# Kernel optimization log

Hardware: AMD Instinct MI355X
Metric: run time of the kernel (lower is better)

## Reference

```python
import jax, jax.numpy as jnp
import numpy as np

DIM = 1024
D_STATE = 16
D_CONV = 4
EXPAND = 2
D_INNER = EXPAND * DIM          # 2048
DT_RANK = -(-DIM // 16)        # ceil(dim/16) = 64
BATCH = 2
SEQ = 1024


def activation_quant(x):
    # int8 fake-quant with STE, per-row scale (matches torch source incl. grad paths)
    scale = 127.0 / jnp.clip(jnp.max(jnp.abs(x), axis=-1, keepdims=True), 1e-5)
    s = x * scale
    q = jnp.clip(jnp.round(s), -128.0, 127.0)
    return (jax.lax.stop_gradient(q - s) + s) / scale


def weight_quant(w):
    # ternary quant {-1,0,1} with straight-through estimator (grad = identity)
    scale = jnp.clip(jnp.mean(jnp.abs(w)), 1e-5)
    wq = jnp.clip(jnp.round(w / scale), -1.0, 1.0)
    return w + jax.lax.stop_gradient(wq - w)


def bit_linear(x, w):
    # LayerNorm (no affine, eps=1e-5) -> act quant -> ternary-weight matmul
    mu = jnp.mean(x, axis=-1, keepdims=True)
    var = jnp.mean((x - mu) ** 2, axis=-1, keepdims=True)
    xn = (x - mu) * jax.lax.rsqrt(var + 1e-5)
    return activation_quant(xn) @ weight_quant(w).T


def rms_norm(x, w, eps=1e-6):
    return w * (x * jax.lax.rsqrt(jnp.mean(x * x, axis=-1, keepdims=True) + eps))


def selective_scan(x, delta, A, Bm, Cm, D, z):
    # x, delta: [b,l,d]; Bm, Cm: [b,l,n]; A: [d,n]; D: [d]; z: [b,l,d]
    def step(h, inp):
        x_t, d_t, B_t, C_t = inp              # [b,d],[b,d],[b,n],[b,n]
        dA = jnp.exp(d_t[:, :, None] * A)     # [b,d,n]
        h = dA * h + d_t[:, :, None] * B_t[:, None, :] * x_t[:, :, None]
        y = jnp.einsum('bdn,bn->bd', h, C_t)
        return h, y

    h0 = jnp.zeros((x.shape[0], A.shape[0], A.shape[1]), x.dtype)
    seq_first = lambda t: jnp.moveaxis(t, 1, 0)
    _, ys = jax.lax.scan(step, h0, (seq_first(x), seq_first(delta), seq_first(Bm), seq_first(Cm)))
    y = jnp.moveaxis(ys, 0, 1) + x * D
    return y * jax.nn.silu(z)


def mamba_forward(hidden_states, rms_w, in_proj_w, x_proj_w, out_proj_w,
                  conv_w, conv_b, dt_proj_w, dt_proj_b, A_log, D):
    b, l, _ = hidden_states.shape
    h = rms_norm(hidden_states, rms_w)
    xz = bit_linear(h, in_proj_w)                      # [b,l,2*d_inner]
    x, z = jnp.split(xz, 2, axis=-1)

    # depthwise causal conv1d + bias
    xc = jnp.moveaxis(x, 1, 2)                         # [b,d_inner,l]
    xc = jax.lax.conv_general_dilated(
        xc, conv_w, window_strides=(1,), padding=[(D_CONV - 1, 0)],
        feature_group_count=D_INNER, dimension_numbers=('NCH', 'OIH', 'NCH'))
    xc = xc + conv_b[None, :, None]
    x = jax.nn.silu(jnp.moveaxis(xc, 1, 2))            # [b,l,d_inner]

    x_dbl = bit_linear(x, x_proj_w)                    # [b,l,dt_rank+2*d_state]
    dt_low, Bm, Cm = jnp.split(x_dbl, [DT_RANK, DT_RANK + D_STATE], axis=-1)
    dt = dt_low @ dt_proj_w.T + dt_proj_b              # dt_proj (with bias)
    # source passes dt_bias=dt_proj.bias again into the fused scan with softplus
    delta = jax.nn.softplus(dt + dt_proj_b)
    A = -jnp.exp(A_log)

    y = selective_scan(x, delta, A, Bm, Cm, D, z)
    out = bit_linear(y, out_proj_w)
    return hidden_states + out


def setup_inputs() -> dict:
    key = jax.random.key(0)
    ks = jax.random.split(key, 8)
    return {
        'hidden_states': jax.random.normal(ks[0], (BATCH, SEQ, DIM), jnp.float32),
        'rms_w': jnp.ones((DIM,), jnp.float32),
        'in_proj_w': jax.random.normal(ks[1], (2 * D_INNER, DIM), jnp.float32) / np.float32(np.sqrt(DIM)),
        'x_proj_w': jax.random.normal(ks[2], (DT_RANK + 2 * D_STATE, D_INNER), jnp.float32) / np.float32(np.sqrt(D_INNER)),
        'out_proj_w': jax.random.normal(ks[3], (DIM, D_INNER), jnp.float32) / np.float32(np.sqrt(D_INNER)),
        'conv_w': jax.random.normal(ks[4], (D_INNER, 1, D_CONV), jnp.float32) * 0.2,
        'conv_b': jnp.zeros((D_INNER,), jnp.float32),
        'dt_proj_w': jax.random.normal(ks[5], (D_INNER, DT_RANK), jnp.float32) / np.float32(np.sqrt(DT_RANK)),
        'dt_proj_b': jax.random.normal(ks[6], (D_INNER,), jnp.float32) * 0.01,
        'A_log': jnp.log(jnp.tile(jnp.arange(1, D_STATE + 1, dtype=jnp.float32), (D_INNER, 1))),
        'D': jnp.ones((D_INNER,), jnp.float32),
    }


def reference(hidden_states, rms_w, in_proj_w, x_proj_w, out_proj_w,
              conv_w, conv_b, dt_proj_w, dt_proj_b, A_log, D):
    return mamba_forward(hidden_states, rms_w, in_proj_w, x_proj_w, out_proj_w,
                         conv_w, conv_b, dt_proj_w, dt_proj_b, A_log, D)
```

## Files before the change

### kernel.cpp

```cpp
#include <hip/hip_runtime.h>
#include <hip/hip_bf16.h>

#define BATCH 2
#define SEQ 1024
#define DIM 1024
#define DINNER 2048
#define NSTATE 16
#define DTRANK 64
#define NDBL 96
#define ROWS (BATCH*SEQ)
#define NC 32
#define TC 32
#define KSPLIT 8

#define N_IN_W  (4096*1024)
#define N_X_W   (NDBL*DINNER)
#define N_OUT_W (1024*2048)

typedef __attribute__((ext_vector_type(8))) short bf16x8;
typedef __attribute__((ext_vector_type(4))) float f32x4;

__device__ inline float wave_sum64(float v){
#pragma unroll
  for (int o=32;o>0;o>>=1) v += __shfl_xor(v,o,64);
  return v;
}
__device__ inline float wave_max64(float v){
#pragma unroll
  for (int o=32;o>0;o>>=1) v = fmaxf(v,__shfl_xor(v,o,64));
  return v;
}
__device__ inline float block_sum256(float v, float* sred){
  v = wave_sum64(v);
  if ((threadIdx.x&63)==0) sred[threadIdx.x>>6]=v;
  __syncthreads();
  float t = sred[0]+sred[1]+sred[2]+sred[3];
  __syncthreads();
  return t;
}
__device__ inline float block_max256(float v, float* sred){
  v = wave_max64(v);
  if ((threadIdx.x&63)==0) sred[threadIdx.x>>6]=v;
  __syncthreads();
  float t = fmaxf(fmaxf(sred[0],sred[1]),fmaxf(sred[2],sred[3]));
  __syncthreads();
  return t;
}

__global__ __launch_bounds__(256) void prelude_k(
    const float* __restrict__ w0, const float* __restrict__ w1,
    const float* __restrict__ w2, float* __restrict__ part,
    const float* __restrict__ hidden, const float* __restrict__ rmsw,
    __hip_bfloat16* __restrict__ q, float* __restrict__ rs,
    float* __restrict__ xdbl_zero)
{
  __shared__ float sred[4];
  const int bid = blockIdx.x, tid = threadIdx.x;
  if (bid < 1536){
    const int wsel = bid >> 9, bx = bid & 511;
    const float* w; int n;
    if (wsel==0){ w=w0; n=N_IN_W; }
    else if (wsel==1){ w=w1; n=N_X_W; }
    else { w=w2; n=N_OUT_W; }
    float s = 0.f;
    for (int i = bx*256 + tid; i < n; i += 512*256) s += fabsf(w[i]);
    s = block_sum256(s, sred);
    if (tid==0) part[wsel*512 + bx] = s;
    return;
  }
  if (bid < 3584){
    const int r = bid - 1536;
    const float* row = hidden + (size_t)r*1024;
    float v[4];
#pragma unroll
    for (int i=0;i<4;i++) v[i] = row[tid + i*256];
    float ss=0.f;
#pragma unroll
    for (int i=0;i<4;i++) ss += v[i]*v[i];
    ss = block_sum256(ss, sred);
    float f = rsqrtf(ss/1024.f + 1e-6f);
#pragma unroll
    for (int i=0;i<4;i++) v[i] *= f * rmsw[tid + i*256];
    float s=0.f;
#pragma unroll
    for (int i=0;i<4;i++) s += v[i];
    s = block_sum256(s, sred);
    const float mu = s/1024.f;
    float vs=0.f;
#pragma unroll
    for (int i=0;i<4;i++){ float d=v[i]-mu; vs += d*d; }
    vs = block_sum256(vs, sred);
    const float inv = rsqrtf(vs/1024.f + 1e-5f);
    float am=0.f;
#pragma unroll
    for (int i=0;i<4;i++){ v[i] = (v[i]-mu)*inv; am = fmaxf(am, fabsf(v[i])); }
    am = block_max256(am, sred);
    am = fmaxf(am, 1e-5f);
    const float scale = 127.f/am;
    if (tid==0) rs[r] = am*(1.f/127.f);
#pragma unroll
    for (int i=0;i<4;i++){
      float qv = fminf(fmaxf(rintf(v[i]*scale), -128.f), 127.f);
      q[(size_t)r*1024 + tid + i*256] = __float2bfloat16(qv);
    }
    return;
  }
  {
    const int idx = (bid - 3584)*256 + tid;
    ((float4*)xdbl_zero)[idx] = (float4){0.f,0.f,0.f,0.f};
  }
}

__device__ inline void tern4(const float* __restrict__ w, ushort* __restrict__ wq,
                             int i, float s){
  const float4 v = ((const float4*)w)[i];
  float q0 = fminf(fmaxf(rintf(v.x/s),-1.f),1.f);
  float q1 = fminf(fmaxf(rintf(v.y/s),-1.f),1.f);
  float q2 = fminf(fmaxf(rintf(v.z/s),-1.f),1.f);
  float q3 = fminf(fmaxf(rintf(v.w/s),-1.f),1.f);
  __hip_bfloat16 h0=__float2bfloat16(q0), h1=__float2bfloat16(q1);
  __hip_bfloat16 h2=__float2bfloat16(q2), h3=__float2bfloat16(q3);
  ushort4 o;
  o.x=*(ushort*)&h0; o.y=*(ushort*)&h1; o.z=*(ushort*)&h2; o.w=*(ushort*)&h3;
  ((ushort4*)wq)[i]=o;
}
__global__ __launch_bounds__(256) void ternarize3b_k(const float* __restrict__ w0,
    const float* __restrict__ w1, const float* __restrict__ w2,
    ushort* __restrict__ q0, ushort* __restrict__ q1, ushort* __restrict__ q2,
    const float* __restrict__ part){
  __shared__ float sred[4];
  float sc[3];
#pragma unroll
  for (int w=0; w<3; w++){
    float s = part[w*512 + threadIdx.x] + part[w*512 + threadIdx.x + 256];
    s = block_sum256(s, sred);
    const float c = (w==0)?(float)N_IN_W:((w==1)?(float)N_X_W:(float)N_OUT_W);
    sc[w] = fmaxf(s/c, 1e-5f);
  }
  const int NQ0 = N_IN_W/4, NQ1 = N_X_W/4, PQ1 = (128*2048 - N_X_W)/4, NQ2 = N_OUT_W/4;
  int i = blockIdx.x*256 + threadIdx.x;
  if (i < NQ0){ tern4(w0, q0, i, sc[0]); return; }
  i -= NQ0;
  if (i < NQ1){ tern4(w1, q1, i, sc[1]); return; }
  i -= NQ1;
  if (i < PQ1){ ((ushort4*)q1)[NQ1 + i] = (ushort4){0,0,0,0}; return; }
  i -= PQ1;
  if (i < NQ2){ tern4(w2, q2, i, sc[2]); }
}

__global__ __launch_bounds__(256) void conv_ln_quant_k(const float* __restrict__ x,
    const float* __restrict__ cw, const float* __restrict__ cb,
    float* __restrict__ xc, __hip_bfloat16* __restrict__ q, float* __restrict__ rs){
  __shared__ float sred[4];
  const int r = blockIdx.x, tid = threadIdx.x;
  const int t = r & (SEQ-1);
  float v[8];
#pragma unroll
  for (int i=0;i<8;i++){
    const int d = tid + i*256;
    const float4 w4 = ((const float4*)cw)[d];
    const float wj[4] = {w4.x, w4.y, w4.z, w4.w};
    float acc = cb[d];
#pragma unroll
    for (int j=0;j<4;j++){
      const int tt = t-3+j;
      if (tt>=0) acc += x[(size_t)(r-3+j)*DINNER + d]*wj[j];
    }
    acc = acc/(1.f+expf(-acc));
    xc[(size_t)r*DINNER + d] = acc;
    v[i] = acc;
  }
  float s=0.f;
#pragma unroll
  for (int i=0;i<8;i++) s += v[i];
  s = block_sum256(s, sred);
  const float mu = s/2048.f;
  float vs=0.f;
#pragma unroll
  for (int i=0;i<8;i++){ float d=v[i]-mu; vs += d*d; }
  vs = block_sum256(vs, sred);
  const float inv = rsqrtf(vs/2048.f + 1e-5f);
  float am=0.f;
#pragma unroll
  for (int i=0;i<8;i++){ v[i] = (v[i]-mu)*inv; am = fmaxf(am, fabsf(v[i])); }
  am = block_max256(am, sred);
  am = fmaxf(am, 1e-5f);
  const float scale = 127.f/am;
  if (tid==0) rs[r] = am*(1.f/127.f);
#pragma unroll
  for (int i=0;i<8;i++){
    float qv = fminf(fmaxf(rintf(v[i]*scale), -128.f), 127.f);
    q[(size_t)r*2048 + tid + i*256] = __float2bfloat16(qv);
  }
}

__global__ __launch_bounds__(256) void ln_quant8_k(const float* __restrict__ src,
    __hip_bfloat16* __restrict__ q, float* __restrict__ rs){
  __shared__ float sred[4];
  const int r = blockIdx.x, tid = threadIdx.x;
  const float* row = src + (size_t)r*2048;
  float v[8];
#pragma unroll
  for (int i=0;i<8;i++) v[i] = row[tid + i*256];
  float s=0.f;
#pragma unroll
  for (int i=0;i<8;i++) s += v[i];
  s = block_sum256(s, sred);
  const float mu = s/2048.f;
  float vs=0.f;
#pragma unroll
  for (int i=0;i<8;i++){ float d=v[i]-mu; vs += d*d; }
  vs = block_sum256(vs, sred);
  const float inv = rsqrtf(vs/2048.f + 1e-5f);
  float am=0.f;
#pragma unroll
  for (int i=0;i<8;i++){ v[i] = (v[i]-mu)*inv; am = fmaxf(am, fabsf(v[i])); }
  am = block_max256(am, sred);
  am = fmaxf(am, 1e-5f);
  const float scale = 127.f/am;
  if (tid==0) rs[r] = am*(1.f/127.f);
#pragma unroll
  for (int i=0;i<8;i++){
    float qv = fminf(fmaxf(rintf(v[i]*scale), -128.f), 127.f);
    q[(size_t)r*2048 + tid + i*256] = __float2bfloat16(qv);
  }
}

template<int BM, int BN, int MODE>
__global__ __launch_bounds__(256) void gemm2_k(
    const short* __restrict__ A, const short* __restrict__ Bw,
    const float* __restrict__ rs, int K, int Ksub, int ldc,
    float* __restrict__ out0, float* __restrict__ out1,
    const float* __restrict__ hid)
{
  constexpr int MF = BM/32;
  constexpr int NF = BN/32;
  constexpr int CA = BM/32;
  constexpr int CB = BN/32;
  __shared__ short lsA[BM*64];
  __shared__ short lsB[BN*64];
  const int tid = threadIdx.x;
  const int w = tid>>6, l = tid&63;
  const int m0 = blockIdx.x*BM, n0 = blockIdx.y*BN;
  const int wr = (w>>1)*(BM/2), wc = (w&1)*(BN/2);
  const int lr = l&15, g = l>>4;
  f32x4 acc[MF][NF];
#pragma unroll
  for (int m=0;m<MF;m++)
#pragma unroll
    for (int n=0;n<NF;n++) acc[m][n] = (f32x4){0.f,0.f,0.f,0.f};

  const size_t KB = (size_t)K*2;
  const char* Ag = (const char*)A + (size_t)m0*KB + (size_t)blockIdx.z*Ksub*2;
  const char* Bg = (const char*)Bw + (size_t)n0*KB + (size_t)blockIdx.z*Ksub*2;

  bf16x8 ra[CA], rb[CB];
#define LDG(kb)                                                                   \
  {                                                                               \
    _Pragma("unroll")                                                             \
    for (int c=0;c<CA;c++){ int o=c*4096+tid*16; int rw=o>>7, cl=o&127;           \
      ra[c] = *(const bf16x8*)(Ag + (size_t)rw*KB + (size_t)(kb)*2 + cl); }       \
    _Pragma("unroll")                                                             \
    for (int c=0;c<CB;c++){ int o=c*4096+tid*16; int rw=o>>7, cl=o&127;           \
      rb[c] = *(const bf16x8*)(Bg + (size_t)rw*KB + (size_t)(kb)*2 + cl); }       \
  }

  LDG(0);
  for (int kb=0; kb<Ksub; kb+=64){
    __syncthreads();
#pragma unroll
    for (int c=0;c<CA;c++){ int o=c*4096+tid*16; int rw=o>>7, sl=(o>>4)&7;
      *(bf16x8*)((char*)lsA + (rw<<7) + ((sl^(rw&7))<<4)) = ra[c]; }
#pragma unroll
    for (int c=0;c<CB;c++){ int o=c*4096+tid*16; int rw=o>>7, sl=(o>>4)&7;
      *(bf16x8*)((char*)lsB + (rw<<7) + ((sl^(rw&7))<<4)) = rb[c]; }
    __syncthreads();
    if (kb + 64 < Ksub) LDG(kb+64);
#pragma unroll
    for (int ks=0;ks<2;ks++){
      bf16x8 af[MF], bb[NF];
#pragma unroll
      for (int m=0;m<MF;m++){ int rw = wr + m*16 + lr;
        af[m] = *(const bf16x8*)((const char*)lsA + (rw<<7) + ((((ks<<2)+g)^(lr&7))<<4)); }
#pragma unroll
      for (int n=0;n<NF;n++){ int rw = wc + n*16 + lr;
        bb[n] = *(const bf16x8*)((const char*)lsB + (rw<<7) + ((((ks<<2)+g)^(lr&7))<<4)); }
#pragma unroll
      for (int m=0;m<MF;m++)
#pragma unroll
        for (int n=0;n<NF;n++)
          acc[m][n] = __builtin_amdgcn_mfma_f32_16x16x32_bf16(af[m], bb[n], acc[m][n], 0, 0, 0);
    }
  }
#undef LDG

#pragma unroll
  for (int m=0;m<MF;m++){
    const int rowb = m0 + wr + m*16 + g*4;
#pragma unroll
    for (int j=0;j<4;j++){
      const int row = rowb + j;
      const float rsv = (MODE==4) ? 1.f : rs[row];
#pragma unroll
      for (int n=0;n<NF;n++){
        const int col = n0 + wc + n*16 + lr;
        const float v = acc[m][n][j]*rsv;
        if (MODE==1){
          if (col < 2048) out0[(size_t)row*2048 + col] = v;
          else            out1[(size_t)row*2048 + (col-2048)] = v;
        } else if (MODE==2){
          const size_t o = (size_t)row*ldc + col;
          out0[o] = hid[o] + v;
        } else {
          if (col < NDBL) atomicAdd(&out0[(size_t)row*NDBL + col], v);
        }
      }
    }
  }
}

#define SXT_S 130
#define SW2_S 66
__global__ __launch_bounds__(256) void dt_delta2_k(const float* __restrict__ xdbl,
    const float* __restrict__ rs,
    const float* __restrict__ W, const float* __restrict__ bias, float* __restrict__ delta){
  __shared__ float sXT[64*SXT_S];
  __shared__ float sW2[64*SW2_S];
  const int tid = threadIdx.x;
  const int r0 = blockIdx.x*128, d0 = blockIdx.y*64;
#pragma unroll
  for (int qit=0;qit<8;qit++){
    const int f4 = qit*256 + tid;
    const int rr = f4>>4, k0 = (f4&15)<<2;
    const float rsv = rs[r0+rr];
    const float4 xv4 = *(const float4*)(xdbl + (size_t)(r0+rr)*NDBL + k0);
    sXT[(k0+0)*SXT_S + rr] = xv4.x*rsv;
    sXT[(k0+1)*SXT_S + rr] = xv4.y*rsv;
    sXT[(k0+2)*SXT_S + rr] = xv4.z*rsv;
    sXT[(k0+3)*SXT_S + rr] = xv4.w*rsv;
  }
#pragma unroll
  for (int qit=0;qit<4;qit++){
    const int f4 = qit*256 + tid;
    const int dd = f4>>4, k0 = (f4&15)<<2;
    const float4 wv4 = *(const float4*)(W + (size_t)(d0+dd)*64 + k0);
    sW2[(k0+0)*SW2_S + dd] = wv4.x;
    sW2[(k0+1)*SW2_S + dd] = wv4.y;
    sW2[(k0+2)*SW2_S + dd] = wv4.z;
    sW2[(k0+3)*SW2_S + dd] = wv4.w;
  }
  __syncthreads();
  const int tx = tid&15, ty = tid>>4;
  float acc[8][4];
#pragma unroll
  for (int i=0;i<8;i++)
#pragma unroll
    for (int j=0;j<4;j++) acc[i][j]=0.f;
  for (int k=0;k<64;k++){
    float xv[8], wv[4];
    *(float2*)&xv[0] = *(const float2*)&sXT[k*SXT_S + ty*8 + 0];
    *(float2*)&xv[2] = *(const float2*)&sXT[k*SXT_S + ty*8 + 2];
    *(float2*)&xv[4] = *(const float2*)&sXT[k*SXT_S + ty*8 + 4];
    *(float2*)&xv[6] = *(const float2*)&sXT[k*SXT_S + ty*8 + 6];
    *(float2*)&wv[0] = *(const float2*)&sW2[k*SW2_S + tx*4 + 0];
    *(float2*)&wv[2] = *(const float2*)&sW2[k*SW2_S + tx*4 + 2];
#pragma unroll
    for (int i=0;i<8;i++)
#pragma unroll
      for (int j=0;j<4;j++) acc[i][j] = fmaf(xv[i], wv[j], acc[i][j]);
  }
  const float4 b4 = *(const float4*)(bias + d0 + tx*4);
  const float b2[4] = {2.f*b4.x, 2.f*b4.y, 2.f*b4.z, 2.f*b4.w};
#pragma unroll
  for (int i=0;i<8;i++){
    const int row = r0 + ty*8 + i;
    float4 o;
    float* op = (float*)&o;
#pragma unroll
    for (int j=0;j<4;j++){
      const float xq = acc[i][j] + b2[j];
      op[j] = (xq>20.f) ? xq : log1pf(expf(xq));
    }
    *(float4*)(delta + (size_t)row*DINNER + d0 + tx*4) = o;
  }
}

__global__ __launch_bounds__(256) void scan1_k(const float* __restrict__ delta,
    const float* __restrict__ xc, const float* __restrict__ xdbl,
    const float* __restrict__ rs,
    const float* __restrict__ A_log, float* __restrict__ hloc, float* __restrict__ Ssum){
  __shared__ float sB[TC][16];
  const int tid = threadIdx.x;
  const int d = blockIdx.x*256 + tid;
  const int c = blockIdx.y, b = blockIdx.z;
  const int row0 = b*SEQ + c*TC;
  for (int i=tid;i<TC*16;i+=256){
    int t=i>>4, j=i&15;
    sB[t][j] = xdbl[(size_t)(row0+t)*NDBL + DTRANK + j] * rs[row0+t];
  }
  __syncthreads();
  float a[16];
  const f32x4* Ap = (const f32x4*)(A_log + (size_t)d*16);
#pragma unroll
  for (int q=0;q<4;q++){
    f32x4 av = Ap[q];
#pragma unroll
    for (int j=0;j<4;j++) a[q*4+j] = -__expf(av[j]);
  }
  float h[16];
#pragma unroll
  for (int n=0;n<16;n++) h[n]=0.f;
  float S = 0.f;
  float dl[4], xv[4];
#pragma unroll
  for (int j=0;j<4;j++){
    dl[j] = delta[(size_t)(row0+j)*DINNER + d];
    xv[j] = xc[(size_t)(row0+j)*DINNER + d];
  }
#pragma unroll
  for (int g0=0; g0<TC/4; g0++){
    float dn[4], xn[4];
    if (g0 < TC/4-1){
#pragma unroll
      for (int j=0;j<4;j++){
        dn[j] = delta[(size_t)(row0+g0*4+4+j)*DINNER + d];
        xn[j] = xc[(size_t)(row0+g0*4+4+j)*DINNER + d];
      }
    }
#pragma unroll
    for (int j=0;j<4;j++){
      const int t = g0*4+j;
      const float dlc = dl[j], xvc = xv[j];
      S += dlc;
      const float dx = dlc*xvc;
#pragma unroll
      for (int n=0;n<16;n++)
        h[n] = fmaf(__expf(dlc*a[n]), h[n], dx*sB[t][n]);
    }
#pragma unroll
    for (int j=0;j<4;j++){ dl[j]=dn[j]; xv[j]=xn[j]; }
  }
  f32x4* hp = (f32x4*)(hloc + ((size_t)(b*NC+c)*DINNER + d)*16);
#pragma unroll
  for (int q=0;q<4;q++){
    f32x4 hv;
#pragma unroll
    for (int j=0;j<4;j++) hv[j]=h[q*4+j];
    hp[q]=hv;
  }
  Ssum[(size_t)(b*NC+c)*DINNER + d] = S;
}

__global__ __launch_bounds__(256) void scan2_k(const float* __restrict__ A_log,
    const float* __restrict__ Ssum, float* __restrict__ hloc){
  const int idx = blockIdx.x*256 + threadIdx.x;
  const int n = idx&15, d = (idx>>4)&(DINNER-1), b = idx>>15;
  const float a = -__expf(A_log[(size_t)d*16+n]);
  float hin = 0.f;
  for (int c=0;c<NC;c++){
    const size_t o = ((size_t)(b*NC+c)*DINNER + d)*16 + n;
    const float t = hloc[o];
    hloc[o] = hin;
    hin = fmaf(__expf(a*Ssum[(size_t)(b*NC+c)*DINNER + d]), hin, t);
  }
}

__global__ __launch_bounds__(256) void scan3_k(const float* __restrict__ delta,
    const float* __restrict__ xc, const float* __restrict__ xdbl,
    const float* __restrict__ rs,
    const float* __restrict__ A_log, const float* __restrict__ Dp,
    const float* __restrict__ hloc, float* __restrict__ zy){
  __shared__ float sBC[TC][32];
  const int tid = threadIdx.x;
  const int d = blockIdx.x*256 + tid;
  const int c = blockIdx.y, b = blockIdx.z;
  const int row0 = b*SEQ + c*TC;
  for (int i=tid;i<TC*32;i+=256){
    int t=i>>5, j=i&31;
    sBC[t][j] = xdbl[(size_t)(row0+t)*NDBL + DTRANK + j] * rs[row0+t];
  }
  __syncthreads();
  float a[16];
  const f32x4* Ap = (const f32x4*)(A_log + (size_t)d*16);
#pragma unroll
  for (int q=0;q<4;q++){
    f32x4 av = Ap[q];
#pragma unroll
    for (int j=0;j<4;j++) a[q*4+j] = -__expf(av[j]);
  }
  float h[16];
  const f32x4* hp = (const f32x4*)(hloc + ((size_t)(b*NC+c)*DINNER + d)*16);
#pragma unroll
  for (int q=0;q<4;q++){
    f32x4 hv = hp[q];
#pragma unroll
    for (int j=0;j<4;j++) h[q*4+j]=hv[j];
  }
  const float Dv = Dp[d];
  float dl[4], xv[4], zv[4];
#pragma unroll
  for (int j=0;j<4;j++){
    dl[j] = delta[(size_t)(row0+j)*DINNER + d];
    xv[j] = xc[(size_t)(row0+j)*DINNER + d];
    zv[j] = zy[(size_t)(row0+j)*DINNER + d];
  }
#pragma unroll
  for (int g0=0; g0<TC/4; g0++){
    float dn[4], xn[4], zn[4];
    if (g0 < TC/4-1){
#pragma unroll
      for (int j=0;j<4;j++){
        dn[j] = delta[(size_t)(row0+g0*4+4+j)*DINNER + d];
        xn[j] = xc[(size_t)(row0+g0*4+4+j)*DINNER + d];
        zn[j] = zy[(size_t)(row0+g0*4+4+j)*DINNER + d];
      }
    }
#pragma unroll
    for (int j=0;j<4;j++){
      const int t = g0*4+j;
      const float dlc = dl[j], xvc = xv[j], zvc = zv[j];
      const float dx = dlc*xvc;
      float p = 0.f;
#pragma unroll
      for (int n=0;n<16;n++){
        h[n] = fmaf(__expf(dlc*a[n]), h[n], dx*sBC[t][n]);
        p = fmaf(h[n], sBC[t][16+n], p);
      }
      float y = p + xvc*Dv;
      y *= zvc/(1.f+__expf(-zvc));
      zy[(size_t)(row0+t)*DINNER + d] = y;
    }
#pragma unroll
    for (int j=0;j<4;j++){ dl[j]=dn[j]; xv[j]=xn[j]; zv[j]=zn[j]; }
  }
}

extern "C" void kernel_launch(void* const* d_in, const int* in_sizes, int n_in,
                              void* d_out, int out_size, void* d_ws, size_t ws_size,
                              hipStream_t stream){
  (void)in_sizes; (void)n_in; (void)out_size; (void)ws_size;
  const float* hidden    = (const float*)d_in[0];
  const float* rms_w     = (const float*)d_in[1];
  const float* in_proj_w = (const float*)d_in[2];
  const float* x_proj_w  = (const float*)d_in[3];
  const float* out_proj_w= (const float*)d_in[4];
  const float* conv_w    = (const float*)d_in[5];
  const float* conv_b    = (const float*)d_in[6];
  const float* dt_proj_w = (const float*)d_in[7];
  const float* dt_proj_b = (const float*)d_in[8];
  const float* A_log     = (const float*)d_in[9];
  const float* Dp        = (const float*)d_in[10];

  char* ws = (char*)d_ws; size_t off = 0;
  auto alloc = [&](size_t b)->void* { void* p = ws + off; off += (b + 255) & ~(size_t)255; return p; };
  float* part3 = (float*)alloc(3*512*4);
  float* RS    = (float*)alloc((size_t)ROWS*4);
  __hip_bfloat16* WQin  = (__hip_bfloat16*)alloc((size_t)4096*1024*2);
  __hip_bfloat16* WQx   = (__hip_bfloat16*)alloc((size_t)128*2048*2);
  __hip_bfloat16* WQout = (__hip_bfloat16*)alloc((size_t)1024*2048*2);
  __hip_bfloat16* QA    = (__hip_bfloat16*)alloc((size_t)ROWS*2048*2);
  float* XBUF  = (float*)alloc((size_t)ROWS*DINNER*4);
  float* ZBUF  = (float*)alloc((size_t)ROWS*DINNER*4);
  float* XC    = (float*)alloc((size_t)ROWS*DINNER*4);
  float* XDBL  = (float*)alloc((size_t)ROWS*NDBL*4);
  float* HLOC  = (float*)alloc((size_t)BATCH*NC*DINNER*16*4);
  float* SSUM  = (float*)alloc((size_t)BATCH*NC*DINNER*4);

  prelude_k<<<3776,256,0,stream>>>(in_proj_w, x_proj_w, out_proj_w, part3,
                                   hidden, rms_w, QA, RS, XDBL);
  {
    const int totq = N_IN_W/4 + 128*2048/4 + N_OUT_W/4;
    ternarize3b_k<<<(totq+255)/256,256,0,stream>>>(in_proj_w, x_proj_w, out_proj_w,
        (ushort*)WQin, (ushort*)WQx, (ushort*)WQout, part3);
  }
  gemm2_k<128,128,1><<<dim3(ROWS/128, 4096/128, 1),256,0,stream>>>((const short*)QA,
      (const short*)WQin, RS, DIM, DIM, 0, XBUF, ZBUF, nullptr);
  conv_ln_quant_k<<<ROWS,256,0,stream>>>(XBUF, conv_w, conv_b, XC, QA, RS);
  gemm2_k<64,128,4><<<dim3(ROWS/64, 1, KSPLIT),256,0,stream>>>((const short*)QA,
      (const short*)WQx, nullptr, DINNER, DINNER/KSPLIT, NDBL, XDBL, nullptr, nullptr);
  dt_delta2_k<<<dim3(ROWS/128, DINNER/64),256,0,stream>>>(XDBL, RS, dt_proj_w, dt_proj_b, XBUF);
  scan1_k<<<dim3(DINNER/256, NC, BATCH),256,0,stream>>>(XBUF, XC, XDBL, RS, A_log, HLOC, SSUM);
  scan2_k<<<(BATCH*DINNER*16)/256,256,0,stream>>>(A_log, SSUM, HLOC);
  scan3_k<<<dim3(DINNER/256, NC, BATCH),256,0,stream>>>(XBUF, XC, XDBL, RS, A_log, Dp, HLOC, ZBUF);
  ln_quant8_k<<<ROWS,256,0,stream>>>(ZBUF, QA, RS);
  gemm2_k<64,64,2><<<dim3(ROWS/64, 1024/64, 1),256,0,stream>>>((const short*)QA,
      (const short*)WQout, RS, DINNER, DINNER, DIM, (float*)d_out, nullptr, hidden);
}
```

Measured before the change: 178.7 us.

## Switch quantized GEMMs from bf16 to int8 MFMA with int8 storage

Quantized activations and ternary weights are now stored as int8 instead of bf16, and all three GEMMs use the i32 16x16x64 int8 MFMA with a 128-wide K tile. This halves the bytes moved for weights and activations and doubles the math per MFMA instruction. Integer accumulation is exact for these value ranges, so the results should stay correct. The K loop runs half as many iterations, and the LDS tile keeps the same byte footprint.

Result: faster. 160.6 us (-10.1%).

```diff
diff --git a/kernel.cpp b/kernel.cpp
--- a/kernel.cpp
+++ b/kernel.cpp
@@ -17,8 +17,8 @@
 #define N_X_W   (NDBL*DINNER)
 #define N_OUT_W (1024*2048)
 
-typedef __attribute__((ext_vector_type(8))) short bf16x8;
 typedef __attribute__((ext_vector_type(4))) float f32x4;
+typedef __attribute__((ext_vector_type(4))) int   i32x4;
 
 __device__ inline float wave_sum64(float v){
 #pragma unroll
@@ -51,7 +51,7 @@
     const float* __restrict__ w0, const float* __restrict__ w1,
     const float* __restrict__ w2, float* __restrict__ part,
     const float* __restrict__ hidden, const float* __restrict__ rmsw,
-    __hip_bfloat16* __restrict__ q, float* __restrict__ rs,
+    char* __restrict__ q, float* __restrict__ rs,
     float* __restrict__ xdbl_zero)
 {
   __shared__ float sred[4];
@@ -101,7 +101,7 @@
 #pragma unroll
     for (int i=0;i<4;i++){
       float qv = fminf(fmaxf(rintf(v[i]*scale), -128.f), 127.f);
-      q[(size_t)r*1024 + tid + i*256] = __float2bfloat16(qv);
+      q[(size_t)r*1024 + tid + i*256] = (char)qv;
     }
     return;
   }
@@ -111,22 +111,19 @@
   }
 }
 
-__device__ inline void tern4(const float* __restrict__ w, ushort* __restrict__ wq,
+__device__ inline void tern4(const float* __restrict__ w, char* __restrict__ wq,
                              int i, float s){
   const float4 v = ((const float4*)w)[i];
-  float q0 = fminf(fmaxf(rintf(v.x/s),-1.f),1.f);
-  float q1 = fminf(fmaxf(rintf(v.y/s),-1.f),1.f);
-  float q2 = fminf(fmaxf(rintf(v.z/s),-1.f),1.f);
-  float q3 = fminf(fmaxf(rintf(v.w/s),-1.f),1.f);
-  __hip_bfloat16 h0=__float2bfloat16(q0), h1=__float2bfloat16(q1);
-  __hip_bfloat16 h2=__float2bfloat16(q2), h3=__float2bfloat16(q3);
-  ushort4 o;
-  o.x=*(ushort*)&h0; o.y=*(ushort*)&h1; o.z=*(ushort*)&h2; o.w=*(ushort*)&h3;
-  ((ushort4*)wq)[i]=o;
+  char4 o;
+  o.x = (char)fminf(fmaxf(rintf(v.x/s),-1.f),1.f);
+  o.y = (char)fminf(fmaxf(rintf(v.y/s),-1.f),1.f);
+  o.z = (char)fminf(fmaxf(rintf(v.z/s),-1.f),1.f);
+  o.w = (char)fminf(fmaxf(rintf(v.w/s),-1.f),1.f);
+  ((char4*)wq)[i]=o;
 }
 __global__ __launch_bounds__(256) void ternarize3b_k(const float* __restrict__ w0,
     const float* __restrict__ w1, const float* __restrict__ w2,
-    ushort* __restrict__ q0, ushort* __restrict__ q1, ushort* __restrict__ q2,
+    char* __restrict__ q0, char* __restrict__ q1, char* __restrict__ q2,
     const float* __restrict__ part){
   __shared__ float sred[4];
   float sc[3];
@@ -143,14 +140,14 @@
   i -= NQ0;
   if (i < NQ1){ tern4(w1, q1, i, sc[1]); return; }
   i -= NQ1;
-  if (i < PQ1){ ((ushort4*)q1)[NQ1 + i] = (ushort4){0,0,0,0}; return; }
+  if (i < PQ1){ char4 z; z.x=z.y=z.z=z.w=0; ((char4*)q1)[NQ1 + i] = z; return; }
   i -= PQ1;
   if (i < NQ2){ tern4(w2, q2, i, sc[2]); }
 }
 
 __global__ __launch_bounds__(256) void conv_ln_quant_k(const float* __restrict__ x,
     const float* __restrict__ cw, const float* __restrict__ cb,
-    float* __restrict__ xc, __hip_bfloat16* __restrict__ q, float* __restrict__ rs){
+    float* __restrict__ xc, char* __restrict__ q, float* __restrict__ rs){
   __shared__ float sred[4];
   const int r = blockIdx.x, tid = threadIdx.x;
   const int t = r & (SEQ-1);
@@ -190,12 +187,12 @@
 #pragma unroll
   for (int i=0;i<8;i++){
     float qv = fminf(fmaxf(rintf(v[i]*scale), -128.f), 127.f);
-    q[(size_t)r*2048 + tid + i*256] = __float2bfloat16(qv);
+    q[(size_t)r*2048 + tid + i*256] = (char)qv;
   }
 }
 
 __global__ __launch_bounds__(256) void ln_quant8_k(const float* __restrict__ src,
-    __hip_bfloat16* __restrict__ q, float* __restrict__ rs){
+    char* __restrict__ q, float* __restrict__ rs){
   __shared__ float sred[4];
   const int r = blockIdx.x, tid = threadIdx.x;
   const float* row = src + (size_t)r*2048;
@@ -222,13 +219,13 @@
 #pragma unroll
   for (int i=0;i<8;i++){
     float qv = fminf(fmaxf(rintf(v[i]*scale), -128.f), 127.f);
-    q[(size_t)r*2048 + tid + i*256] = __float2bfloat16(qv);
+    q[(size_t)r*2048 + tid + i*256] = (char)qv;
   }
 }
 
 template<int BM, int BN, int MODE>
 __global__ __launch_bounds__(256) void gemm2_k(
-    const short* __restrict__ A, const short* __restrict__ Bw,
+    const char* __restrict__ A, const char* __restrict__ Bw,
     const float* __restrict__ rs, int K, int Ksub, int ldc,
     float* __restrict__ out0, float* __restrict__ out1,
     const float* __restrict__ hid)
@@ -237,59 +234,59 @@
   constexpr int NF = BN/32;
   constexpr int CA = BM/32;
   constexpr int CB = BN/32;
-  __shared__ short lsA[BM*64];
-  __shared__ short lsB[BN*64];
+  __shared__ char lsA[BM*128];
+  __shared__ char lsB[BN*128];
   const int tid = threadIdx.x;
   const int w = tid>>6, l = tid&63;
   const int m0 = blockIdx.x*BM, n0 = blockIdx.y*BN;
   const int wr = (w>>1)*(BM/2), wc = (w&1)*(BN/2);
   const int lr = l&15, g = l>>4;
-  f32x4 acc[MF][NF];
+  i32x4 acc[MF][NF];
 #pragma unroll
   for (int m=0;m<MF;m++)
 #pragma unroll
-    for (int n=0;n<NF;n++) acc[m][n] = (f32x4){0.f,0.f,0.f,0.f};
-
-  const size_t KB = (size_t)K*2;
-  const char* Ag = (const char*)A + (size_t)m0*KB + (size_t)blockIdx.z*Ksub*2;
-  const char* Bg = (const char*)Bw + (size_t)n0*KB + (size_t)blockIdx.z*Ksub*2;
-
-  bf16x8 ra[CA], rb[CB];
+    for (int n=0;n<NF;n++) acc[m][n] = (i32x4){0,0,0,0};
+
+  const size_t KB = (size_t)K;
+  const char* Ag = A + (size_t)m0*KB + (size_t)blockIdx.z*Ksub;
+  const char* Bg = Bw + (size_t)n0*KB + (size_t)blockIdx.z*Ksub;
+
+  i32x4 ra[CA], rb[CB];
 #define LDG(kb)                                                                   \
   {                                                                               \
     _Pragma("unroll")                                                             \
     for (int c=0;c<CA;c++){ int o=c*4096+tid*16; int rw=o>>7, cl=o&127;           \
-      ra[c] = *(const bf16x8*)(Ag + (size_t)rw*KB + (size_t)(kb)*2 + cl); }       \
+      ra[c] = *(const i32x4*)(Ag + (size_t)rw*KB + (size_t)(kb) + cl); }          \
     _Pragma("unroll")                                                             \
     for (int c=0;c<CB;c++){ int o=c*4096+tid*16; int rw=o>>7, cl=o&127;           \
-      rb[c] = *(const bf16x8*)(Bg + (size_t)rw*KB + (size_t)(kb)*2 + cl); }       \
+      rb[c] = *(const i32x4*)(Bg + (size_t)rw*KB + (size_t)(kb) + cl); }          \
   }
 
   LDG(0);
-  for (int kb=0; kb<Ksub; kb+=64){
+  for (int kb=0; kb<Ksub; kb+=128){
     __syncthreads();
 #pragma unroll
     for (int c=0;c<CA;c++){ int o=c*4096+tid*16; int rw=o>>7, sl=(o>>4)&7;
-      *(bf16x8*)((char*)lsA + (rw<<7) + ((sl^(rw&7))<<4)) = ra[c]; }
+      *(i32x4*)(lsA + (rw<<7) + ((sl^(rw&7))<<4)) = ra[c]; }
 #pragma unroll
     for (int c=0;c<CB;c++){ int o=c*4096+tid*16; int rw=o>>7, sl=(o>>4)&7;
-      *(bf16x8*)((char*)lsB + (rw<<7) + ((sl^(rw&7))<<4)) = rb[c]; }
+      *(i32x4*)(lsB + (rw<<7) + ((sl^(rw&7))<<4)) = rb[c]; }
     __syncthreads();
-    if (kb + 64 < Ksub) LDG(kb+64);
+    if (kb + 128 < Ksub) LDG(kb+128);
 #pragma unroll
     for (int ks=0;ks<2;ks++){
-      bf16x8 af[MF], bb[NF];
+      i32x4 af[MF], bb[NF];
 #pragma unroll
       for (int m=0;m<MF;m++){ int rw = wr + m*16 + lr;
-        af[m] = *(const bf16x8*)((const char*)lsA + (rw<<7) + ((((ks<<2)+g)^(lr&7))<<4)); }
+        af[m] = *(const i32x4*)(lsA + (rw<<7) + ((((ks<<2)+g)^(lr&7))<<4)); }
 #pragma unroll
       for (int n=0;n<NF;n++){ int rw = wc + n*16 + lr;
-        bb[n] = *(const bf16x8*)((const char*)lsB + (rw<<7) + ((((ks<<2)+g)^(lr&7))<<4)); }
+        bb[n] = *(const i32x4*)(lsB + (rw<<7) + ((((ks<<2)+g)^(lr&7))<<4)); }
 #pragma unroll
       for (int m=0;m<MF;m++)
 #pragma unroll
         for (int n=0;n<NF;n++)
-          acc[m][n] = __builtin_amdgcn_mfma_f32_16x16x32_bf16(af[m], bb[n], acc[m][n], 0, 0, 0);
+          acc[m][n] = __builtin_amdgcn_mfma_i32_16x16x64_i8(af[m], bb[n], acc[m][n], 0, 0, 0);
     }
   }
 #undef LDG
@@ -304,7 +301,7 @@
 #pragma unroll
       for (int n=0;n<NF;n++){
         const int col = n0 + wc + n*16 + lr;
-        const float v = acc[m][n][j]*rsv;
+        const float v = (float)acc[m][n][j]*rsv;
         if (MODE==1){
           if (col < 2048) out0[(size_t)row*2048 + col] = v;
           else            out1[(size_t)row*2048 + (col-2048)] = v;
@@ -555,10 +552,10 @@
   auto alloc = [&](size_t b)->void* { void* p = ws + off; off += (b + 255) & ~(size_t)255; return p; };
   float* part3 = (float*)alloc(3*512*4);
   float* RS    = (float*)alloc((size_t)ROWS*4);
-  __hip_bfloat16* WQin  = (__hip_bfloat16*)alloc((size_t)4096*1024*2);
-  __hip_bfloat16* WQx   = (__hip_bfloat16*)alloc((size_t)128*2048*2);
-  __hip_bfloat16* WQout = (__hip_bfloat16*)alloc((size_t)1024*2048*2);
-  __hip_bfloat16* QA    = (__hip_bfloat16*)alloc((size_t)ROWS*2048*2);
+  char* WQin   = (char*)alloc((size_t)4096*1024);
+  char* WQx    = (char*)alloc((size_t)128*2048);
+  char* WQout  = (char*)alloc((size_t)1024*2048);
+  char* QA     = (char*)alloc((size_t)ROWS*2048);
   float* XBUF  = (float*)alloc((size_t)ROWS*DINNER*4);
   float* ZBUF  = (float*)alloc((size_t)ROWS*DINNER*4);
   float* XC    = (float*)alloc((size_t)ROWS*DINNER*4);
@@ -571,18 +568,18 @@
   {
     const int totq = N_IN_W/4 + 128*2048/4 + N_OUT_W/4;
     ternarize3b_k<<<(totq+255)/256,256,0,stream>>>(in_proj_w, x_proj_w, out_proj_w,
-        (ushort*)WQin, (ushort*)WQx, (ushort*)WQout, part3);
-  }
-  gemm2_k<128,128,1><<<dim3(ROWS/128, 4096/128, 1),256,0,stream>>>((const short*)QA,
-      (const short*)WQin, RS, DIM, DIM, 0, XBUF, ZBUF, nullptr);
+        WQin, WQx, WQout, part3);
+  }
+  gemm2_k<128,128,1><<<dim3(ROWS/128, 4096/128, 1),256,0,stream>>>(QA, WQin,
+      RS, DIM, DIM, 0, XBUF, ZBUF, nullptr);
   conv_ln_quant_k<<<ROWS,256,0,stream>>>(XBUF, conv_w, conv_b, XC, QA, RS);
-  gemm2_k<64,128,4><<<dim3(ROWS/64, 1, KSPLIT),256,0,stream>>>((const short*)QA,
-      (const short*)WQx, nullptr, DINNER, DINNER/KSPLIT, NDBL, XDBL, nullptr, nullptr);
+  gemm2_k<64,128,4><<<dim3(ROWS/64, 1, KSPLIT),256,0,stream>>>(QA, WQx,
+      nullptr, DINNER, DINNER/KSPLIT, NDBL, XDBL, nullptr, nullptr);
   dt_delta2_k<<<dim3(ROWS/128, DINNER/64),256,0,stream>>>(XDBL, RS, dt_proj_w, dt_proj_b, XBUF);
   scan1_k<<<dim3(DINNER/256, NC, BATCH),256,0,stream>>>(XBUF, XC, XDBL, RS, A_log, HLOC, SSUM);
   scan2_k<<<(BATCH*DINNER*16)/256,256,0,stream>>>(A_log, SSUM, HLOC);
   scan3_k<<<dim3(DINNER/256, NC, BATCH),256,0,stream>>>(XBUF, XC, XDBL, RS, A_log, Dp, HLOC, ZBUF);
   ln_quant8_k<<<ROWS,256,0,stream>>>(ZBUF, QA, RS);
-  gemm2_k<64,64,2><<<dim3(ROWS/64, 1024/64, 1),256,0,stream>>>((const short*)QA,
-      (const short*)WQout, RS, DINNER, DINNER, DIM, (float*)d_out, nullptr, hidden);
-}
+  gemm2_k<64,64,2><<<dim3(ROWS/64, 1024/64, 1),256,0,stream>>>(QA, WQout,
+      RS, DINNER, DINNER, DIM, (float*)d_out, nullptr, hidden);
+}
```
